# Kernel optimization log

Measured on AMD Instinct MI355X. Metric: run time of the kernel, lower is better.

## Reference

```python
import jax, jax.numpy as jnp
import numpy as np

HEADS = 16
EMBED = 1024
D_K = EMBED // HEADS


def setup_inputs() -> dict:
    key = jax.random.key(0)
    ks = jax.random.split(key, 11)
    B, S, E = 4, 2048, EMBED
    sc = 0.02
    return {
        "query": jax.random.normal(ks[0], (B, S, E), jnp.float32),
        "key_": jax.random.normal(ks[1], (B, S, E), jnp.float32),
        "value": jax.random.normal(ks[2], (B, S, E), jnp.float32),
        "Wq": jax.random.normal(ks[3], (E, E), jnp.float32) * sc,
        "bq": jnp.zeros((E,), jnp.float32),
        "Wk": jax.random.normal(ks[4], (E, E), jnp.float32) * sc,
        "bk": jnp.zeros((E,), jnp.float32),
        "Wv": jax.random.normal(ks[5], (E, E), jnp.float32) * sc,
        "bv": jnp.zeros((E,), jnp.float32),
        "Wo": jax.random.normal(ks[6], (E, D_K), jnp.float32) * sc,  # out: Linear(heads*d_k -> d_k)
        "bo": jnp.zeros((D_K,), jnp.float32),
    }


def reference(query, key_, value, Wq, bq, Wk, bk, Wv, bv, Wo, bo):
    B, S, E = query.shape
    H, Dk = HEADS, D_K
    # QKV projections
    q = query @ Wq + bq          # (B,S,E)
    k = key_ @ Wk + bk
    v = value @ Wv + bv
    # split heads -> (B,H,S,Dk)
    q = q.reshape(B, S, H, Dk).transpose(0, 2, 1, 3)
    k = k.reshape(B, S, H, Dk).transpose(0, 2, 1, 3)
    v = v.reshape(B, S, H, Dk).transpose(0, 2, 1, 3)
    # attention: softmax(QK^T / sqrt(d_k)) V
    scores = jnp.einsum("bhqd,bhkd->bhqk", q, k) / jnp.sqrt(jnp.asarray(Dk, q.dtype))
    attn = jax.nn.softmax(scores, axis=-1)
    ctx = jnp.einsum("bhqk,bhkd->bhqd", attn, v)
    ctx = ctx.transpose(0, 2, 1, 3).reshape(B, S, E)
    # output projection (E -> d_k, as in source)
    return ctx @ Wo + bo
```

## Files before the change

kernel.cpp:

```cpp
#include <hip/hip_runtime.h>
#include <hip/hip_bf16.h>
#include <cstdint>
#include <cstddef>

#define DEVI static __device__ __forceinline__

typedef unsigned short u16;
typedef unsigned int u32;
typedef __bf16 bf16_t;
typedef __bf16 bf16x8 __attribute__((ext_vector_type(8)));
typedef float f32x4 __attribute__((ext_vector_type(4)));
typedef float f32x16 __attribute__((ext_vector_type(16)));

union U16x8 { uint4 u; bf16x8 v; };
union PU { u32 w[4]; bf16x8 v; };

#define QSCALE 0.1803368801111204f

DEVI void gload_lds16(const void* g, void* l) {
  __builtin_amdgcn_global_load_lds((const __attribute__((address_space(1))) void*)g,
                                   (__attribute__((address_space(3))) void*)l, 16, 0, 0);
}
DEVI void wait_vmcnt0() { asm volatile("s_waitcnt vmcnt(0)" ::: "memory"); }

DEVI u32 pack2(float a, float b) {
  u16 x = __builtin_bit_cast(u16, (bf16_t)a);
  u16 y = __builtin_bit_cast(u16, (bf16_t)b);
  return (u32)x | ((u32)y << 16);
}

DEVI u32 cvt_pk_bf16(float lo, float hi) {
  u32 r;
  asm("v_cvt_pk_bf16_f32 %0, %1, %2" : "=v"(r) : "v"(lo), "v"(hi));
  return r;
}

DEVI void permswap(u32& a, u32& b) {
  asm("v_permlane32_swap_b32 %0, %1" : "+v"(a), "+v"(b));
}

DEVI f32x16 mfma32(bf16x8 a, bf16x8 b, f32x16 c) {
  return __builtin_amdgcn_mfma_f32_32x32x16_bf16(a, b, c, 0, 0, 0);
}

DEVI bf16x8 lds_frag(const char* base, int row, int koff, int swz) {
  U16x8 u;
  u.u = *(const uint4*)(base + row * 128 + (koff ^ swz));
  return u.v;
}

__global__ __launch_bounds__(256) void k_cvt3(
    const float* __restrict__ a, const float* __restrict__ b, const float* __restrict__ c,
    bf16_t* __restrict__ dst) {
  int which = blockIdx.x >> 10;
  int bb = blockIdx.x & 1023;
  const float* s = which == 0 ? a : which == 1 ? b : c;
  u16* d = (u16*)dst + (size_t)which * 8192 * 1024;
  size_t base = ((size_t)bb * 256 + threadIdx.x) * 8;
  #pragma unroll
  for (int p = 0; p < 4; ++p) {
    size_t i = base + (size_t)p * 2097152;
    float4 f0 = *(const float4*)(s + i);
    float4 f1 = *(const float4*)(s + i + 4);
    uint4 o;
    o.x = cvt_pk_bf16(f0.x, f0.y); o.y = cvt_pk_bf16(f0.z, f0.w);
    o.z = cvt_pk_bf16(f1.x, f1.y); o.w = cvt_pk_bf16(f1.z, f1.w);
    *(uint4*)(d + i) = o;
  }
}

__global__ __launch_bounds__(256) void k_transpose_convert(
    const float* __restrict__ src, bf16_t* __restrict__ dst, int R, int C, float scale) {
  int tiles_c = C >> 6;
  int tc = blockIdx.x % tiles_c;
  int tr = blockIdx.x / tiles_c;
  int r0 = tr << 6, c0 = tc << 6;
  __shared__ u16 tile[64][65];
  int t = threadIdx.x;
  #pragma unroll
  for (int p = 0; p < 4; ++p) {
    int idx = t + p * 256;
    int i = idx >> 4, j4 = (idx & 15) * 4;
    float4 f = *(const float4*)(src + (size_t)(r0 + i) * C + c0 + j4);
    tile[i][j4 + 0] = __builtin_bit_cast(u16, (bf16_t)(f.x * scale));
    tile[i][j4 + 1] = __builtin_bit_cast(u16, (bf16_t)(f.y * scale));
    tile[i][j4 + 2] = __builtin_bit_cast(u16, (bf16_t)(f.z * scale));
    tile[i][j4 + 3] = __builtin_bit_cast(u16, (bf16_t)(f.w * scale));
  }
  __syncthreads();
  #pragma unroll
  for (int p = 0; p < 2; ++p) {
    int idx = t + p * 256;
    int j = idx >> 3, i0 = (idx & 7) * 8;
    u16 us[8];
    #pragma unroll
    for (int e = 0; e < 8; ++e) us[e] = tile[i0 + e][j];
    uint4 o;
    o.x = (u32)us[0] | ((u32)us[1] << 16);
    o.y = (u32)us[2] | ((u32)us[3] << 16);
    o.z = (u32)us[4] | ((u32)us[5] << 16);
    o.w = (u32)us[6] | ((u32)us[7] << 16);
    *(uint4*)((u16*)dst + (size_t)(c0 + j) * R + r0 + i0) = o;
  }
}

template<bool PRE>
__global__ __launch_bounds__(256) void k_proj_gemm(
    const float* __restrict__ Aq, const float* __restrict__ Ak, const float* __restrict__ Av,
    const bf16_t* __restrict__ Abf,
    const bf16_t* __restrict__ WqT, const bf16_t* __restrict__ WkT, const bf16_t* __restrict__ WvT,
    const float* __restrict__ bq, const float* __restrict__ bk, const float* __restrict__ bv,
    bf16_t* __restrict__ qh, bf16_t* __restrict__ kh, bf16_t* __restrict__ vh) {
  int bx = blockIdx.x;
  int which = bx >> 9;
  int tt = bx & 511;
  int tile_m = tt & 63;
  int tile_n = tt >> 6;
  const float* A    = which == 0 ? Aq : which == 1 ? Ak : Av;
  const bf16_t* Ab  = Abf + (size_t)which * 8192 * 1024;
  const bf16_t* WT  = which == 0 ? WqT : which == 1 ? WkT : WvT;
  const float* bias = which == 0 ? bq : which == 1 ? bk : bv;
  const float bscale = which == 0 ? QSCALE : 1.0f;
  bf16_t* dst       = which == 0 ? qh : which == 1 ? kh : vh;

  const int t = threadIdx.x;
  const int l = t & 63;
  const int w = t >> 6;
  const int wm = w >> 1, wn = w & 1;
  const int c = l & 15, g = l >> 4;
  const int row0 = tile_m << 7;
  const int n0 = tile_n << 7;

  __shared__ __align__(16) char As[128 * 64 * 2];
  __shared__ __align__(16) char Bs[128 * 64 * 2];

  f32x4 acc[4][4];
  #pragma unroll
  for (int i = 0; i < 4; ++i)
    #pragma unroll
    for (int j = 0; j < 4; ++j) acc[i][j] = (f32x4){0.f, 0.f, 0.f, 0.f};

  const int arow_b = t >> 4, ac4 = t & 15;
  const float* agbase = A + (size_t)(row0 + arow_b) * 1024 + ac4 * 4;
  char* aldst = As + arow_b * 128 + (((ac4 >> 1) ^ (arow_b & 7)) << 4) + (ac4 & 1) * 8;

  for (int kt = 0; kt < 16; ++kt) {
    __syncthreads();
    if constexpr (PRE) {
      #pragma unroll
      for (int cc = 0; cc < 4; ++cc) {
        int slot = w * 256 + cc * 64 + l;
        int row = slot >> 3, chs = slot & 7;
        const bf16_t* src = Ab + (size_t)(row0 + row) * 1024 + kt * 64 + ((chs ^ (row & 7)) << 3);
        gload_lds16(src, As + (w * 256 + cc * 64) * 16);
      }
    } else {
      const float* ap = agbase + kt * 64;
      #pragma unroll
      for (int p = 0; p < 8; ++p) {
        float4 f = *(const float4*)(ap + (size_t)p * 16384);
        uint2 o;
        o.x = cvt_pk_bf16(f.x, f.y);
        o.y = cvt_pk_bf16(f.z, f.w);
        *(uint2*)(aldst + p * 2048) = o;
      }
    }
    #pragma unroll
    for (int cc = 0; cc < 4; ++cc) {
      int slot = w * 256 + cc * 64 + l;
      int row = slot >> 3, chs = slot & 7;
      const bf16_t* src = WT + (size_t)(n0 + row) * 1024 + kt * 64 + ((chs ^ (row & 7)) << 3);
      gload_lds16(src, Bs + (w * 256 + cc * 64) * 16);
    }
    wait_vmcnt0();
    __syncthreads();
    #pragma unroll
    for (int kk = 0; kk < 2; ++kk) {
      bf16x8 af[4], bfr[4];
      #pragma unroll
      for (int mi = 0; mi < 4; ++mi) {
        int row = wm * 64 + mi * 16 + c;
        U16x8 u; u.u = *(const uint4*)(As + row * 128 + ((kk * 64 + g * 16) ^ ((c & 7) << 4)));
        af[mi] = u.v;
      }
      #pragma unroll
      for (int ni = 0; ni < 4; ++ni) {
        int row = wn * 64 + ni * 16 + c;
        U16x8 u; u.u = *(const uint4*)(Bs + row * 128 + ((kk * 64 + g * 16) ^ ((c & 7) << 4)));
        bfr[ni] = u.v;
      }
      #pragma unroll
      for (int mi = 0; mi < 4; ++mi)
        #pragma unroll
        for (int ni = 0; ni < 4; ++ni)
          acc[mi][ni] = __builtin_amdgcn_mfma_f32_16x16x32_bf16(af[mi], bfr[ni], acc[mi][ni], 0, 0, 0);
    }
  }
  u16* dd = (u16*)dst;
  #pragma unroll
  for (int ni = 0; ni < 4; ++ni) {
    int col = n0 + wn * 64 + ni * 16 + c;
    float bb = bias[col] * bscale;
    int h = col >> 6, d = col & 63;
    #pragma unroll
    for (int mi = 0; mi < 4; ++mi) {
      #pragma unroll
      for (int r = 0; r < 4; ++r) {
        int rowg = row0 + wm * 64 + mi * 16 + g * 4 + r;
        int b = rowg >> 11, s = rowg & 2047;
        float vv = acc[mi][ni][r] + bb;
        size_t idx = (((size_t)b * 16 + h) * 2048 + s) * 64 + d;
        dd[idx] = __builtin_bit_cast(u16, (bf16_t)vv);
      }
    }
  }
}

__global__ __launch_bounds__(256) void k_transpose_v(
    const bf16_t* __restrict__ vh, bf16_t* __restrict__ vT) {
  int bh = blockIdx.x >> 5, st = blockIdx.x & 31;
  int s0 = st << 6;
  __shared__ __align__(16) u16 tile[64][72];
  int t = threadIdx.x;
  const u16* src = (const u16*)vh + ((size_t)bh * 2048 + s0) * 64;
  #pragma unroll
  for (int p = 0; p < 2; ++p) {
    int idx = t + p * 256;
    int s = idx >> 3, d0 = (idx & 7) * 8;
    uint4 v = *(const uint4*)(src + s * 64 + d0);
    *(uint4*)(&tile[s][d0]) = v;
  }
  __syncthreads();
  u16* dst = (u16*)vT + (size_t)bh * 64 * 2048 + s0;
  #pragma unroll
  for (int p = 0; p < 2; ++p) {
    int idx = t + p * 256;
    int d = idx >> 3, s1 = (idx & 7) * 8;
    u16 us[8];
    #pragma unroll
    for (int e = 0; e < 8; ++e) us[e] = tile[s1 + e][d];
    uint4 o;
    o.x = (u32)us[0] | ((u32)us[1] << 16);
    o.y = (u32)us[2] | ((u32)us[3] << 16);
    o.z = (u32)us[4] | ((u32)us[5] << 16);
    o.w = (u32)us[6] | ((u32)us[7] << 16);
    *(uint4*)(dst + (size_t)d * 2048 + s1) = o;
  }
}

__global__ __launch_bounds__(256, 4) void k_attn(
    const bf16_t* __restrict__ qh, const bf16_t* __restrict__ kh,
    const bf16_t* __restrict__ vT, bf16_t* __restrict__ ctx) {
  const int bid = blockIdx.x;
  const int bx = ((bid & 7) << 7) | (bid >> 3);
  const int bh = bx >> 4;
  const int qt = bx & 15;
  const int q0 = qt << 7;
  const int t = threadIdx.x, l = t & 63, w = t >> 6;
  const int q = l & 31;
  const int hi = l >> 5;
  const int swz = (q & 7) << 4;

  __shared__ __align__(16) char Ks[2][64 * 128];
  __shared__ __align__(16) char Vs[2][64 * 128];
  __shared__ __align__(16) float Dn[4][32];

  const u16* qrow = (const u16*)qh + ((size_t)bh * 2048 + q0 + w * 32 + q) * 64;
  bf16x8 qf0, qf1, qf2, qf3;
  {
    U16x8 u;
    u.u = *(const uint4*)(qrow + 0 * 16 + hi * 8); qf0 = u.v;
    u.u = *(const uint4*)(qrow + 1 * 16 + hi * 8); qf1 = u.v;
    u.u = *(const uint4*)(qrow + 2 * 16 + hi * 8); qf2 = u.v;
    u.u = *(const uint4*)(qrow + 3 * 16 + hi * 8); qf3 = u.v;
  }

  const f32x16 z16 = {0.f,0.f,0.f,0.f, 0.f,0.f,0.f,0.f, 0.f,0.f,0.f,0.f, 0.f,0.f,0.f,0.f};
  f32x16 oc0 = z16, oc1 = z16;
  float l_run = 0.f;

  const u16* kbh = (const u16*)kh + (size_t)bh * 2048 * 64;
  const u16* vbh = (const u16*)vT + (size_t)bh * 64 * 2048;

  auto stage = [&](int kvi, int buf) {
    int kbase = kvi << 6;
    #pragma unroll
    for (int cc = 0; cc < 2; ++cc) {
      int slot = w * 128 + cc * 64 + l;
      int row = slot >> 3, chs = slot & 7;
      gload_lds16(kbh + (size_t)(kbase + row) * 64 + ((chs ^ (row & 7)) << 3),
                  Ks[buf] + (w * 128 + cc * 64) * 16);
      gload_lds16(vbh + (size_t)row * 2048 + kbase + ((chs ^ (row & 7)) << 3),
                  Vs[buf] + (w * 128 + cc * 64) * 16);
    }
  };

  stage(0, 0);
  wait_vmcnt0();
  __syncthreads();

  for (int kv = 0; kv < 32; ++kv) {
    const int cur = kv & 1;
    if (kv < 31) stage(kv + 1, cur ^ 1);
    const char* Kc = Ks[cur];
    const char* Vc = Vs[cur];

    #pragma unroll
    for (int tt = 0; tt < 2; ++tt) {
      const int arow = tt * 32 + q;
      f32x16 st = z16;
      __builtin_amdgcn_s_setprio(1);
      st = mfma32(lds_frag(Kc, arow, 0 * 32 + hi * 16, swz), qf0, st);
      st = mfma32(lds_frag(Kc, arow, 1 * 32 + hi * 16, swz), qf1, st);
      st = mfma32(lds_frag(Kc, arow, 2 * 32 + hi * 16, swz), qf2, st);
      st = mfma32(lds_frag(Kc, arow, 3 * 32 + hi * 16, swz), qf3, st);
      __builtin_amdgcn_s_setprio(0);

      float e[16];
      #pragma unroll
      for (int i = 0; i < 16; ++i) {
        e[i] = __builtin_amdgcn_exp2f(st[i]);
        l_run += e[i];
      }

      #pragma unroll
      for (int cc = 0; cc < 2; ++cc) {
        u32 a  = cvt_pk_bf16(e[8 * cc + 0], e[8 * cc + 1]);
        u32 b  = cvt_pk_bf16(e[8 * cc + 4], e[8 * cc + 5]);
        u32 c2 = cvt_pk_bf16(e[8 * cc + 2], e[8 * cc + 3]);
        u32 d  = cvt_pk_bf16(e[8 * cc + 6], e[8 * cc + 7]);
        permswap(a, b);
        permswap(c2, d);
        PU pu;
        pu.w[0] = a; pu.w[1] = c2; pu.w[2] = b; pu.w[3] = d;
        const int ks = tt * 2 + cc;
        __builtin_amdgcn_s_setprio(1);
        oc0 = mfma32(pu.v, lds_frag(Vc, q,      ks * 32 + hi * 16, swz), oc0);
        oc1 = mfma32(pu.v, lds_frag(Vc, 32 + q, ks * 32 + hi * 16, swz), oc1);
        __builtin_amdgcn_s_setprio(0);
      }
    }
    wait_vmcnt0();
    __syncthreads();
  }

  l_run += __shfl_xor(l_run, 32);
  Dn[w][q] = 1.f / l_run;
  __syncthreads();

  const int b = bh >> 4, hh = bh & 15;
  u16* cb = (u16*)ctx;
  #pragma unroll
  for (int qd = 0; qd < 4; ++qd) {
    float4 dv = *(const float4*)&Dn[w][qd * 8 + hi * 4];
    #pragma unroll
    for (int r = 0; r < 4; ++r) {
      float inv = (&dv.x)[r];
      int qrow_g = q0 + w * 32 + qd * 8 + hi * 4 + r;
      size_t base = ((size_t)b * 2048 + qrow_g) * 1024 + hh * 64;
      float v0 = oc0[qd * 4 + r] * inv;
      float v1 = oc1[qd * 4 + r] * inv;
      cb[base + q]      = __builtin_bit_cast(u16, (bf16_t)v0);
      cb[base + 32 + q] = __builtin_bit_cast(u16, (bf16_t)v1);
    }
  }
}

__global__ __launch_bounds__(256) void k_out_gemm(
    const bf16_t* __restrict__ ctx, const bf16_t* __restrict__ WoT,
    const float* __restrict__ bo, float* __restrict__ out) {
  int tile_m = blockIdx.x;
  const int t = threadIdx.x, l = t & 63, w = t >> 6;
  const int wm = w >> 1, wn = w & 1;
  const int c = l & 15, g = l >> 4;
  const int row0 = tile_m << 7;

  __shared__ __align__(16) char As[128 * 64 * 2];
  __shared__ __align__(16) char Bs[64 * 64 * 2];

  f32x4 acc[4][2];
  #pragma unroll
  for (int i = 0; i < 4; ++i)
    #pragma unroll
    for (int j = 0; j < 2; ++j) acc[i][j] = (f32x4){0.f, 0.f, 0.f, 0.f};

  for (int kt = 0; kt < 16; ++kt) {
    __syncthreads();
    #pragma unroll
    for (int cc = 0; cc < 4; ++cc) {
      int slot = w * 256 + cc * 64 + l;
      int row = slot >> 3, chs = slot & 7;
      const bf16_t* src = ctx + (size_t)(row0 + row) * 1024 + kt * 64 + ((chs ^ (row & 7)) << 3);
      gload_lds16(src, As + (w * 256 + cc * 64) * 16);
    }
    #pragma unroll
    for (int cc = 0; cc < 2; ++cc) {
      int slot = w * 128 + cc * 64 + l;
      int row = slot >> 3, chs = slot & 7;
      const bf16_t* src = WoT + (size_t)row * 1024 + kt * 64 + ((chs ^ (row & 7)) << 3);
      gload_lds16(src, Bs + (w * 128 + cc * 64) * 16);
    }
    wait_vmcnt0();
    __syncthreads();
    #pragma unroll
    for (int kk = 0; kk < 2; ++kk) {
      bf16x8 af[4], bfr[2];
      #pragma unroll
      for (int mi = 0; mi < 4; ++mi) {
        int row = wm * 64 + mi * 16 + c;
        U16x8 u; u.u = *(const uint4*)(As + row * 128 + ((kk * 64 + g * 16) ^ ((c & 7) << 4)));
        af[mi] = u.v;
      }
      #pragma unroll
      for (int ni = 0; ni < 2; ++ni) {
        int row = wn * 32 + ni * 16 + c;
        U16x8 u; u.u = *(const uint4*)(Bs + row * 128 + ((kk * 64 + g * 16) ^ ((c & 7) << 4)));
        bfr[ni] = u.v;
      }
      #pragma unroll
      for (int mi = 0; mi < 4; ++mi)
        #pragma unroll
        for (int ni = 0; ni < 2; ++ni)
          acc[mi][ni] = __builtin_amdgcn_mfma_f32_16x16x32_bf16(af[mi], bfr[ni], acc[mi][ni], 0, 0, 0);
    }
  }
  #pragma unroll
  for (int ni = 0; ni < 2; ++ni) {
    int col = wn * 32 + ni * 16 + c;
    float bb = bo[col];
    #pragma unroll
    for (int mi = 0; mi < 4; ++mi) {
      #pragma unroll
      for (int r = 0; r < 4; ++r) {
        int rowg = row0 + wm * 64 + mi * 16 + g * 4 + r;
        out[(size_t)rowg * 64 + col] = acc[mi][ni][r] + bb;
      }
    }
  }
}

extern "C" void kernel_launch(void* const* d_in, const int* in_sizes, int n_in,
                              void* d_out, int out_size, void* d_ws, size_t ws_size,
                              hipStream_t stream) {
  (void)in_sizes; (void)n_in; (void)out_size;
  const float* query = (const float*)d_in[0];
  const float* key_  = (const float*)d_in[1];
  const float* value = (const float*)d_in[2];
  const float* Wq = (const float*)d_in[3];
  const float* bq = (const float*)d_in[4];
  const float* Wk = (const float*)d_in[5];
  const float* bk = (const float*)d_in[6];
  const float* Wv = (const float*)d_in[7];
  const float* bv = (const float*)d_in[8];
  const float* Wo = (const float*)d_in[9];
  const float* bo = (const float*)d_in[10];
  float* out = (float*)d_out;

  char* ws = (char*)d_ws;
  bf16_t* WqT = (bf16_t*)(ws + (size_t)0);
  bf16_t* WkT = (bf16_t*)(ws + ((size_t)2 << 20));
  bf16_t* WvT = (bf16_t*)(ws + ((size_t)4 << 20));
  bf16_t* WoT = (bf16_t*)(ws + ((size_t)6 << 20));
  bf16_t* qhd = (bf16_t*)(ws + ((size_t)8 << 20));
  bf16_t* khd = (bf16_t*)(ws + ((size_t)24 << 20));
  bf16_t* vhd = (bf16_t*)(ws + ((size_t)40 << 20));
  bf16_t* vT  = (bf16_t*)(ws + ((size_t)56 << 20));
  bf16_t* ctx = (bf16_t*)(ws + ((size_t)72 << 20));
  bf16_t* Abf = (bf16_t*)(ws + ((size_t)88 << 20));

  const bool pre = ws_size >= ((size_t)137 << 20);

  k_transpose_convert<<<256, 256, 0, stream>>>(Wq, WqT, 1024, 1024, QSCALE);
  k_transpose_convert<<<256, 256, 0, stream>>>(Wk, WkT, 1024, 1024, 1.0f);
  k_transpose_convert<<<256, 256, 0, stream>>>(Wv, WvT, 1024, 1024, 1.0f);
  k_transpose_convert<<<16, 256, 0, stream>>>(Wo, WoT, 1024, 64, 1.0f);

  if (pre) {
    k_cvt3<<<3072, 256, 0, stream>>>(query, key_, value, Abf);
    k_proj_gemm<true><<<1536, 256, 0, stream>>>(query, key_, value, Abf, WqT, WkT, WvT,
                                                bq, bk, bv, qhd, khd, vhd);
  } else {
    k_proj_gemm<false><<<1536, 256, 0, stream>>>(query, key_, value, Abf, WqT, WkT, WvT,
                                                 bq, bk, bv, qhd, khd, vhd);
  }
  k_transpose_v<<<2048, 256, 0, stream>>>(vhd, vT);
  k_attn<<<1024, 256, 0, stream>>>(qhd, khd, vT, ctx);
  k_out_gemm<<<64, 256, 0, stream>>>(ctx, WoT, bo, out);
}
```

Before: 204.7 us.

## Merge prep kernels into one launch and compute softmax denominators via MFMA

```diff
diff --git a/kernel.cpp b/kernel.cpp
--- a/kernel.cpp
+++ b/kernel.cpp
@@ -23,12 +23,6 @@
 }
 DEVI void wait_vmcnt0() { asm volatile("s_waitcnt vmcnt(0)" ::: "memory"); }
 
-DEVI u32 pack2(float a, float b) {
-  u16 x = __builtin_bit_cast(u16, (bf16_t)a);
-  u16 y = __builtin_bit_cast(u16, (bf16_t)b);
-  return (u32)x | ((u32)y << 16);
-}
-
 DEVI u32 cvt_pk_bf16(float lo, float hi) {
   u32 r;
   asm("v_cvt_pk_bf16_f32 %0, %1, %2" : "=v"(r) : "v"(lo), "v"(hi));
@@ -49,43 +43,22 @@
   return u.v;
 }
 
-__global__ __launch_bounds__(256) void k_cvt3(
-    const float* __restrict__ a, const float* __restrict__ b, const float* __restrict__ c,
-    bf16_t* __restrict__ dst) {
-  int which = blockIdx.x >> 10;
-  int bb = blockIdx.x & 1023;
-  const float* s = which == 0 ? a : which == 1 ? b : c;
-  u16* d = (u16*)dst + (size_t)which * 8192 * 1024;
-  size_t base = ((size_t)bb * 256 + threadIdx.x) * 8;
-  #pragma unroll
-  for (int p = 0; p < 4; ++p) {
-    size_t i = base + (size_t)p * 2097152;
-    float4 f0 = *(const float4*)(s + i);
-    float4 f1 = *(const float4*)(s + i + 4);
-    uint4 o;
-    o.x = cvt_pk_bf16(f0.x, f0.y); o.y = cvt_pk_bf16(f0.z, f0.w);
-    o.z = cvt_pk_bf16(f1.x, f1.y); o.w = cvt_pk_bf16(f1.z, f1.w);
-    *(uint4*)(d + i) = o;
-  }
-}
-
-__global__ __launch_bounds__(256) void k_transpose_convert(
-    const float* __restrict__ src, bf16_t* __restrict__ dst, int R, int C, float scale) {
+DEVI void transpose_body(const float* __restrict__ src, bf16_t* __restrict__ dst,
+                         int R, int C, float scale, int tile, int t,
+                         u16 (*tileb)[65]) {
   int tiles_c = C >> 6;
-  int tc = blockIdx.x % tiles_c;
-  int tr = blockIdx.x / tiles_c;
+  int tc = tile % tiles_c;
+  int tr = tile / tiles_c;
   int r0 = tr << 6, c0 = tc << 6;
-  __shared__ u16 tile[64][65];
-  int t = threadIdx.x;
   #pragma unroll
   for (int p = 0; p < 4; ++p) {
     int idx = t + p * 256;
     int i = idx >> 4, j4 = (idx & 15) * 4;
     float4 f = *(const float4*)(src + (size_t)(r0 + i) * C + c0 + j4);
-    tile[i][j4 + 0] = __builtin_bit_cast(u16, (bf16_t)(f.x * scale));
-    tile[i][j4 + 1] = __builtin_bit_cast(u16, (bf16_t)(f.y * scale));
-    tile[i][j4 + 2] = __builtin_bit_cast(u16, (bf16_t)(f.z * scale));
-    tile[i][j4 + 3] = __builtin_bit_cast(u16, (bf16_t)(f.w * scale));
+    tileb[i][j4 + 0] = __builtin_bit_cast(u16, (bf16_t)(f.x * scale));
+    tileb[i][j4 + 1] = __builtin_bit_cast(u16, (bf16_t)(f.y * scale));
+    tileb[i][j4 + 2] = __builtin_bit_cast(u16, (bf16_t)(f.z * scale));
+    tileb[i][j4 + 3] = __builtin_bit_cast(u16, (bf16_t)(f.w * scale));
   }
   __syncthreads();
   #pragma unroll
@@ -94,13 +67,48 @@
     int j = idx >> 3, i0 = (idx & 7) * 8;
     u16 us[8];
     #pragma unroll
-    for (int e = 0; e < 8; ++e) us[e] = tile[i0 + e][j];
+    for (int e = 0; e < 8; ++e) us[e] = tileb[i0 + e][j];
     uint4 o;
     o.x = (u32)us[0] | ((u32)us[1] << 16);
     o.y = (u32)us[2] | ((u32)us[3] << 16);
     o.z = (u32)us[4] | ((u32)us[5] << 16);
     o.w = (u32)us[6] | ((u32)us[7] << 16);
     *(uint4*)((u16*)dst + (size_t)(c0 + j) * R + r0 + i0) = o;
+  }
+}
+
+__global__ __launch_bounds__(256) void k_prep(
+    const float* __restrict__ qa, const float* __restrict__ ka, const float* __restrict__ va,
+    const float* __restrict__ Wq, const float* __restrict__ Wk,
+    const float* __restrict__ Wv, const float* __restrict__ Wo,
+    bf16_t* __restrict__ Abf,
+    bf16_t* __restrict__ WqT, bf16_t* __restrict__ WkT,
+    bf16_t* __restrict__ WvT, bf16_t* __restrict__ WoT) {
+  __shared__ u16 tileb[64][65];
+  const int bid = blockIdx.x;
+  const int t = threadIdx.x;
+  if (bid < 3072) {
+    int which = bid >> 10;
+    int bb = bid & 1023;
+    const float* s = which == 0 ? qa : which == 1 ? ka : va;
+    u16* d = (u16*)Abf + (size_t)which * 8192 * 1024;
+    size_t base = ((size_t)bb * 256 + t) * 8;
+    #pragma unroll
+    for (int p = 0; p < 4; ++p) {
+      size_t i = base + (size_t)p * 2097152;
+      float4 f0 = *(const float4*)(s + i);
+      float4 f1 = *(const float4*)(s + i + 4);
+      uint4 o;
+      o.x = cvt_pk_bf16(f0.x, f0.y); o.y = cvt_pk_bf16(f0.z, f0.w);
+      o.z = cvt_pk_bf16(f1.x, f1.y); o.w = cvt_pk_bf16(f1.z, f1.w);
+      *(uint4*)(d + i) = o;
+    }
+  } else {
+    int r = bid - 3072;
+    if (r < 256)      transpose_body(Wq, WqT, 1024, 1024, QSCALE, r,       t, tileb);
+    else if (r < 512) transpose_body(Wk, WkT, 1024, 1024, 1.0f,   r - 256, t, tileb);
+    else if (r < 768) transpose_body(Wv, WvT, 1024, 1024, 1.0f,   r - 512, t, tileb);
+    else              transpose_body(Wo, WoT, 1024, 64,   1.0f,   r - 768, t, tileb);
   }
 }
 
@@ -263,7 +271,6 @@
 
   __shared__ __align__(16) char Ks[2][64 * 128];
   __shared__ __align__(16) char Vs[2][64 * 128];
-  __shared__ __align__(16) float Dn[4][32];
 
   const u16* qrow = (const u16*)qh + ((size_t)bh * 2048 + q0 + w * 32 + q) * 64;
   bf16x8 qf0, qf1, qf2, qf3;
@@ -275,9 +282,15 @@
     u.u = *(const uint4*)(qrow + 3 * 16 + hi * 8); qf3 = u.v;
   }
 
+  bf16x8 ones;
+  {
+    U16x8 u;
+    u.u = (uint4){0x3F803F80u, 0x3F803F80u, 0x3F803F80u, 0x3F803F80u};
+    ones = u.v;
+  }
+
   const f32x16 z16 = {0.f,0.f,0.f,0.f, 0.f,0.f,0.f,0.f, 0.f,0.f,0.f,0.f, 0.f,0.f,0.f,0.f};
-  f32x16 oc0 = z16, oc1 = z16;
-  float l_run = 0.f;
+  f32x16 oc0 = z16, oc1 = z16, psum = z16;
 
   const u16* kbh = (const u16*)kh + (size_t)bh * 2048 * 64;
   const u16* vbh = (const u16*)vT + (size_t)bh * 64 * 2048;
@@ -318,10 +331,7 @@
 
       float e[16];
       #pragma unroll
-      for (int i = 0; i < 16; ++i) {
-        e[i] = __builtin_amdgcn_exp2f(st[i]);
-        l_run += e[i];
-      }
+      for (int i = 0; i < 16; ++i) e[i] = __builtin_amdgcn_exp2f(st[i]);
 
       #pragma unroll
       for (int cc = 0; cc < 2; ++cc) {
@@ -337,6 +347,7 @@
         __builtin_amdgcn_s_setprio(1);
         oc0 = mfma32(pu.v, lds_frag(Vc, q,      ks * 32 + hi * 16, swz), oc0);
         oc1 = mfma32(pu.v, lds_frag(Vc, 32 + q, ks * 32 + hi * 16, swz), oc1);
+        psum = mfma32(pu.v, ones, psum);
         __builtin_amdgcn_s_setprio(0);
       }
     }
@@ -344,18 +355,13 @@
     __syncthreads();
   }
 
-  l_run += __shfl_xor(l_run, 32);
-  Dn[w][q] = 1.f / l_run;
-  __syncthreads();
-
   const int b = bh >> 4, hh = bh & 15;
   u16* cb = (u16*)ctx;
   #pragma unroll
   for (int qd = 0; qd < 4; ++qd) {
-    float4 dv = *(const float4*)&Dn[w][qd * 8 + hi * 4];
     #pragma unroll
     for (int r = 0; r < 4; ++r) {
-      float inv = (&dv.x)[r];
+      float inv = 1.f / psum[qd * 4 + r];
       int qrow_g = q0 + w * 32 + qd * 8 + hi * 4 + r;
       size_t base = ((size_t)b * 2048 + qrow_g) * 1024 + hh * 64;
       float v0 = oc0[qd * 4 + r] * inv;
@@ -470,16 +476,14 @@
 
   const bool pre = ws_size >= ((size_t)137 << 20);
 
-  k_transpose_convert<<<256, 256, 0, stream>>>(Wq, WqT, 1024, 1024, QSCALE);
-  k_transpose_convert<<<256, 256, 0, stream>>>(Wk, WkT, 1024, 1024, 1.0f);
-  k_transpose_convert<<<256, 256, 0, stream>>>(Wv, WvT, 1024, 1024, 1.0f);
-  k_transpose_convert<<<16, 256, 0, stream>>>(Wo, WoT, 1024, 64, 1.0f);
-
   if (pre) {
-    k_cvt3<<<3072, 256, 0, stream>>>(query, key_, value, Abf);
+    k_prep<<<3856, 256, 0, stream>>>(query, key_, value, Wq, Wk, Wv, Wo,
+                                     Abf, WqT, WkT, WvT, WoT);
     k_proj_gemm<true><<<1536, 256, 0, stream>>>(query, key_, value, Abf, WqT, WkT, WvT,
                                                 bq, bk, bv, qhd, khd, vhd);
   } else {
+    k_prep<<<3856, 256, 0, stream>>>(query, key_, value, Wq, Wk, Wv, Wo,
+                                     Abf, WqT, WkT, WvT, WoT);
     k_proj_gemm<false><<<1536, 256, 0, stream>>>(query, key_, value, Abf, WqT, WkT, WvT,
                                                  bq, bk, bv, qhd, khd, vhd);
   }
```

Measured after the change: 194.7 us. 4.9% less time.
